# Kernel optimization log

Measured on AMD Instinct MI355X. Metric: run time of the kernel, lower is better.

The kernel has to match this reference:

```python
import jax, jax.numpy as jnp
import numpy as np

B, A, H, D, K = 131072, 6, 256, 128, 512
BETA = 0.25
VQ_LOSS_WEIGHT = 1.0


def setup_inputs() -> dict:
    key = jax.random.key(0)
    ks = jax.random.split(key, 16)
    s = 0.05
    inp = {
        "action": jax.random.normal(ks[0], (B, A), jnp.float32),
        # encoder: Linear(A,H)+ReLU, Linear(H,H)+ReLU, Linear(H,D)
        "enc1_w": jax.random.normal(ks[1], (H, A), jnp.float32) * s,
        "enc1_b": jnp.zeros((H,), jnp.float32),
        "enc2_w": jax.random.normal(ks[2], (H, H), jnp.float32) * s,
        "enc2_b": jnp.zeros((H,), jnp.float32),
        "mu_w": jax.random.normal(ks[3], (D, H), jnp.float32) * s,
        "mu_b": jnp.zeros((D,), jnp.float32),
        # VQ codebook, uniform(-1/K, 1/K) as in torch init
        "emb": jax.random.uniform(ks[4], (K, D), jnp.float32, -1.0 / K, 1.0 / K),
        # decoder: Linear(D,H)+ReLU, Linear(H,H)+ReLU, Linear(H,A)+Tanh
        "dec1_w": jax.random.normal(ks[5], (H, D), jnp.float32) * s,
        "dec1_b": jnp.zeros((H,), jnp.float32),
        "dec2_w": jax.random.normal(ks[6], (H, H), jnp.float32) * s,
        "dec2_b": jnp.zeros((H,), jnp.float32),
        "rec_w": jax.random.normal(ks[7], (A, H), jnp.float32) * s,
        "rec_b": jnp.zeros((A,), jnp.float32),
    }
    return inp


def _lin(x, w, b):
    return x @ w.T + b


def reference(action, enc1_w, enc1_b, enc2_w, enc2_b, mu_w, mu_b, emb,
              dec1_w, dec1_b, dec2_w, dec2_b, rec_w, rec_b):
    sg = jax.lax.stop_gradient
    # encoder MLP -> (B, D)
    h = jax.nn.relu(_lin(action, enc1_w, enc1_b))
    h = jax.nn.relu(_lin(h, enc2_w, enc2_b))
    enc = _lin(h, mu_w, mu_b)
    # VQ: argmin over squared L2 distance (same argmin as torch.cdist p=2)
    d2 = (jnp.sum(enc * enc, axis=1, keepdims=True)
          - 2.0 * (enc @ emb.T)
          + jnp.sum(emb * emb, axis=1))  # (B, K)
    idx = jnp.argmin(d2, axis=-1)  # (B,)
    q = emb[idx]  # (B, D) gather == onehot @ emb
    commitment_loss = jnp.mean((enc - sg(q)) ** 2)
    embedding_loss = jnp.mean((q - sg(enc)) ** 2)
    vq_loss = BETA * commitment_loss + embedding_loss
    # straight-through estimator
    q_st = enc + sg(q - enc)
    # decoder MLP (decode_action_head + decode_common + recons_action_head)
    h = jax.nn.relu(_lin(q_st, dec1_w, dec1_b))
    h = jax.nn.relu(_lin(h, dec2_w, dec2_b))
    recons = jnp.tanh(_lin(h, rec_w, rec_b))
    recons_loss = jnp.mean((recons - action) ** 2)
    total_loss = recons_loss + VQ_LOSS_WEIGHT * vq_loss
    return idx, q_st, total_loss
```

## Files before the change

kernel.cpp:

```cpp
#include <hip/hip_runtime.h>
#include <hip/hip_bf16.h>

#define NB 131072
#define MARGINF 2e-6f
#define WS_E2 256
#define WS_MASK 768
#define WS_MASKW 4096
#define WS_BASE_BYTES ((768 + 4096) * 4)
#define WS_SPLIT_F 4864
#define OFF_W2 0
#define OFF_W3 131072
#define OFF_EMB 196608
#define OFF_D1 327680
#define OFF_D2 393216
#define OFF_RW 524288
#define SPLIT_TOTAL 532480

typedef __attribute__((ext_vector_type(8))) short short8v;
typedef __attribute__((ext_vector_type(4))) float f32x4;
typedef __attribute__((ext_vector_type(4))) unsigned short ushort4v;

#define SWC(j) ((((j) >> 2) & 7) << 2)

__device__ __forceinline__ unsigned short bf16rn(float x) {
    unsigned u = __float_as_uint(x);
    unsigned r = u + 0x7fffu + ((u >> 16) & 1u);
    return (unsigned short)(r >> 16);
}
__device__ __forceinline__ void split2(float x, unsigned short& h, unsigned short& l) {
    h = bf16rn(x);
    float hf = __uint_as_float((unsigned)h << 16);
    l = bf16rn(x - hf);
}

__global__ void prep_kernel(
    const float* __restrict__ w2, const float* __restrict__ w3,
    const float* __restrict__ emb, const float* __restrict__ d1w,
    const float* __restrict__ d2w, const float* __restrict__ rw,
    float* __restrict__ ws, int do_splits)
{
    const int total = 512 + 266240;
    unsigned short* wsb = (unsigned short*)(ws + WS_SPLIT_F);
    for (int idx = blockIdx.x * 256 + threadIdx.x; idx < total; idx += gridDim.x * 256) {
        if (idx < 512) {
            const float* e = emb + (size_t)idx * 128;
            float s0 = 0.f, s1 = 0.f, s2 = 0.f, s3 = 0.f;
            for (int d = 0; d < 128; d += 4) {
                s0 += e[d] * e[d];     s1 += e[d + 1] * e[d + 1];
                s2 += e[d + 2] * e[d + 2]; s3 += e[d + 3] * e[d + 3];
            }
            ws[WS_E2 + idx] = (s0 + s1) + (s2 + s3);
            continue;
        }
        if (!do_splits) continue;
        int j = idx - 512;
        int base, K, o, k;
        float src;
        if (j < 65536) {
            o = j >> 8; k = j & 255; base = OFF_W2; K = 256; src = w2[o * 256 + k];
        } else if (j < 98304) {
            j -= 65536; o = j >> 8; k = j & 255; base = OFF_W3; K = 256; src = w3[o * 256 + k];
        } else if (j < 163840) {
            j -= 98304; o = j >> 7; k = j & 127; base = OFF_EMB; K = 128; src = emb[o * 128 + k];
        } else if (j < 196608) {
            j -= 163840; o = j >> 7; k = j & 127; base = OFF_D1; K = 128; src = d1w[o * 128 + k];
        } else if (j < 262144) {
            j -= 196608; o = j >> 8; k = j & 255; base = OFF_D2; K = 256; src = d2w[o * 256 + k];
        } else {
            j -= 262144; o = j >> 8; k = j & 255; base = OFF_RW; K = 256;
            src = (o < 6) ? rw[o * 256 + k] : 0.f;
        }
        unsigned short h, l;
        split2(src, h, l);
        int jt = o >> 4, c = k >> 5;
        int lane = (((k >> 3) & 3) << 4) | (o & 15);
        int e = k & 7;
        int a = base + ((jt * (K >> 5) + c) * 2) * 512 + lane * 8 + e;
        wsb[a] = h;
        wsb[a + 512] = l;
    }
}


template<int NJT, int KC, bool RELU, bool SQSUM>
__device__ __forceinline__ void mfma_mlp4(
    const short8v* __restrict__ Wf, const float* __restrict__ bias,
    unsigned short* HHp, unsigned short* HLp, float* ENC2Wp,
    int w, int lane)
{
    const int lc = lane & 15, lg = lane >> 4;
    f32x4 acc[NJT][4];
#pragma unroll
    for (int jj = 0; jj < NJT; ++jj)
#pragma unroll
        for (int rt = 0; rt < 4; ++rt)
            acc[jj][rt] = (f32x4){0.f, 0.f, 0.f, 0.f};

    __syncthreads();
    for (int c = 0; c < KC; ++c) {
        const int boff = c * 32 + lg * 8;
        short8v bh[4], bl[4];
#pragma unroll
        for (int rt = 0; rt < 4; ++rt) {
            bh[rt] = *(const short8v*)&HHp[(rt * 16 + lc) * 264 + boff];
            bl[rt] = *(const short8v*)&HLp[(rt * 16 + lc) * 264 + boff];
        }
#pragma unroll
        for (int jj = 0; jj < NJT; ++jj) {
            int fi = (((w * NJT + jj) * KC + c) * 2) * 64 + lane;
            short8v ah = Wf[fi];
            short8v al = Wf[fi + 64];
#pragma unroll
            for (int rt = 0; rt < 4; ++rt) {
                acc[jj][rt] = __builtin_amdgcn_mfma_f32_16x16x32_bf16(al, bh[rt], acc[jj][rt], 0, 0, 0);
                acc[jj][rt] = __builtin_amdgcn_mfma_f32_16x16x32_bf16(ah, bl[rt], acc[jj][rt], 0, 0, 0);
                acc[jj][rt] = __builtin_amdgcn_mfma_f32_16x16x32_bf16(ah, bh[rt], acc[jj][rt], 0, 0, 0);
            }
        }
    }
    __syncthreads();

    float sq[4] = {0.f, 0.f, 0.f, 0.f};
#pragma unroll
    for (int jj = 0; jj < NJT; ++jj) {
        int j0 = (w * NJT + jj) * 16 + lg * 4;
        float4 bv = *(const float4*)&bias[j0];
        float bb[4] = {bv.x, bv.y, bv.z, bv.w};
#pragma unroll
        for (int rt = 0; rt < 4; ++rt) {
            int r = rt * 16 + lc;
            ushort4v hv, lv;
#pragma unroll
            for (int reg = 0; reg < 4; ++reg) {
                float v = acc[jj][rt][reg] + bb[reg];
                if (RELU) v = fmaxf(v, 0.f);
                if (SQSUM) sq[rt] += v * v;
                unsigned short h, l;
                split2(v, h, l);
                hv[reg] = h; lv[reg] = l;
            }
            *(ushort4v*)&HHp[r * 264 + j0] = hv;
            *(ushort4v*)&HLp[r * 264 + j0] = lv;
        }
    }
    if (SQSUM) {
#pragma unroll
        for (int rt = 0; rt < 4; ++rt) {
            float s = sq[rt];
            s += __shfl_xor(s, 16);
            s += __shfl_xor(s, 32);
            if (lg == 0) ENC2Wp[w * 64 + rt * 16 + lc] = s;
        }
    }
}

__global__ __launch_bounds__(256, 2) void vqvae_main_mfma(
    const float* __restrict__ action,
    const float* __restrict__ w1, const float* __restrict__ b1,
    const float* __restrict__ b2, const float* __restrict__ b3,
    const float* __restrict__ emb,
    const float* __restrict__ d1b, const float* __restrict__ d2b,
    const float* __restrict__ rb,
    float* __restrict__ out, float* __restrict__ ws)
{
    extern __shared__ __align__(16) unsigned short DYN[];
    unsigned short* HH = DYN;
    unsigned short* HL = DYN + 64 * 264;

    __shared__ float AT[64 * 6];
    __shared__ float E2S[512];
    __shared__ float TOPV[4][64][3];
    __shared__ float ENC2W[4 * 64];
    __shared__ int IDXR[64];
    __shared__ int FLAGR[64];
    __shared__ float RED[8];

    const int t = threadIdx.x;
    const int w = t >> 6, lane = t & 63;
    const int lc = lane & 15, lg = lane >> 4;
    const int row0 = blockIdx.x * 64;
    const unsigned short* wsb = (const unsigned short*)(ws + WS_SPLIT_F);
    const short8v* W2f = (const short8v*)wsb + OFF_W2 / 8;
    const short8v* W3f = (const short8v*)wsb + OFF_W3 / 8;
    const short8v* EMBf = (const short8v*)wsb + OFF_EMB / 8;
    const short8v* D1f = (const short8v*)wsb + OFF_D1 / 8;
    const short8v* D2f = (const short8v*)wsb + OFF_D2 / 8;
    const short8v* RWf = (const short8v*)wsb + OFF_RW / 8;

    for (int i = t; i < 384; i += 256) AT[i] = action[(size_t)row0 * 6 + i];
    for (int i = t; i < 512; i += 256) E2S[i] = ws[WS_E2 + i];
    __syncthreads();

    {
        float wr[6];
#pragma unroll
        for (int i = 0; i < 6; ++i) wr[i] = w1[t * 6 + i];
        float bb = b1[t];
        for (int r = 0; r < 64; ++r) {
            float s = bb;
#pragma unroll
            for (int i = 0; i < 6; ++i) s += wr[i] * AT[r * 6 + i];
            s = fmaxf(s, 0.f);
            unsigned short h, l;
            split2(s, h, l);
            HH[r * 264 + t] = h;
            HL[r * 264 + t] = l;
        }
    }

    mfma_mlp4<4, 8, true, false>(W2f, b2, HH, HL, ENC2W, w, lane);
    mfma_mlp4<2, 8, false, true>(W3f, b3, HH, HL, ENC2W, w, lane);

    float lvq = 0.f, lrec = 0.f;
    {
        float v1[4][4], v2[4][4];
        int k1r[4][4];
#pragma unroll
        for (int rt = 0; rt < 4; ++rt)
#pragma unroll
            for (int reg = 0; reg < 4; ++reg) {
                v1[rt][reg] = 1e30f; v2[rt][reg] = 1e30f; k1r[rt][reg] = 0;
            }
        __syncthreads();
#pragma unroll
        for (int p = 0; p < 2; ++p) {
            f32x4 vacc[4][4];
#pragma unroll
            for (int kt = 0; kt < 4; ++kt)
#pragma unroll
                for (int rt = 0; rt < 4; ++rt)
                    vacc[kt][rt] = (f32x4){0.f, 0.f, 0.f, 0.f};
            for (int c = 0; c < 4; ++c) {
                const int aoff = c * 32 + lg * 8;
                short8v ah[4], al[4];
#pragma unroll
                for (int rt = 0; rt < 4; ++rt) {
                    ah[rt] = *(const short8v*)&HH[(rt * 16 + lc) * 264 + aoff];
                    al[rt] = *(const short8v*)&HL[(rt * 16 + lc) * 264 + aoff];
                }
#pragma unroll
                for (int kt = 0; kt < 4; ++kt) {
                    int ktg = w * 8 + p * 4 + kt;
                    int fi = ((ktg * 4 + c) * 2) * 64 + lane;
                    short8v bh = EMBf[fi];
                    short8v bl = EMBf[fi + 64];
#pragma unroll
                    for (int rt = 0; rt < 4; ++rt) {
                        vacc[kt][rt] = __builtin_amdgcn_mfma_f32_16x16x32_bf16(al[rt], bh, vacc[kt][rt], 0, 0, 0);
                        vacc[kt][rt] = __builtin_amdgcn_mfma_f32_16x16x32_bf16(ah[rt], bl, vacc[kt][rt], 0, 0, 0);
                        vacc[kt][rt] = __builtin_amdgcn_mfma_f32_16x16x32_bf16(ah[rt], bh, vacc[kt][rt], 0, 0, 0);
                    }
                }
            }
#pragma unroll
            for (int kt = 0; kt < 4; ++kt) {
                int k = (w * 8 + p * 4 + kt) * 16 + lc;
                float ek = E2S[k];
#pragma unroll
                for (int rt = 0; rt < 4; ++rt)
#pragma unroll
                    for (int reg = 0; reg < 4; ++reg) {
                        float dd = ek - 2.f * vacc[kt][rt][reg];
                        if (dd < v1[rt][reg]) {
                            v2[rt][reg] = v1[rt][reg]; v1[rt][reg] = dd; k1r[rt][reg] = k;
                        } else if (dd < v2[rt][reg]) v2[rt][reg] = dd;
                    }
            }
        }
        __syncthreads();

#pragma unroll
        for (int m = 1; m < 16; m <<= 1) {
#pragma unroll
            for (int rt = 0; rt < 4; ++rt)
#pragma unroll
                for (int reg = 0; reg < 4; ++reg) {
                    float ov1 = __shfl_xor(v1[rt][reg], m);
                    int ok1 = __shfl_xor(k1r[rt][reg], m);
                    float ov2 = __shfl_xor(v2[rt][reg], m);
                    if (ov1 < v1[rt][reg] ||
                        (ov1 == v1[rt][reg] && ok1 < k1r[rt][reg])) {
                        v2[rt][reg] = fminf(v1[rt][reg], ov2);
                        v1[rt][reg] = ov1; k1r[rt][reg] = ok1;
                    } else {
                        v2[rt][reg] = fminf(v2[rt][reg], ov1);
                    }
                }
        }
        if (lc == 0) {
#pragma unroll
            for (int rt = 0; rt < 4; ++rt)
#pragma unroll
                for (int reg = 0; reg < 4; ++reg) {
                    int row = rt * 16 + lg * 4 + reg;
                    TOPV[w][row][0] = v1[rt][reg];
                    TOPV[w][row][1] = __int_as_float(k1r[rt][reg]);
                    TOPV[w][row][2] = v2[rt][reg];
                }
        }
    }
    __syncthreads();

    if (t < 64) {
        float v1 = 1e30f, v2 = 1e30f; int k1 = 0;
#pragma unroll
        for (int ww = 0; ww < 4; ++ww) {
            float ov1 = TOPV[ww][t][0];
            int ok1 = __float_as_int(TOPV[ww][t][1]);
            float ov2 = TOPV[ww][t][2];
            if (ov1 < v1 || (ov1 == v1 && ok1 < k1)) {
                v2 = fminf(v1, ov2); v1 = ov1; k1 = ok1;
            } else {
                v2 = fminf(v2, ov1);
            }
        }
        int flag = (v2 - v1 >= MARGINF) ? 0 : 1;
        IDXR[t] = k1;
        FLAGR[t] = flag;
        int row = row0 + t;
        if (flag)
            atomicOr((unsigned int*)ws + WS_MASK + (row >> 5), 1u << (row & 31));
        out[row] = (float)k1;
        if (!flag) {
            float enc2 = ENC2W[0 * 64 + t] + ENC2W[1 * 64 + t] +
                         ENC2W[2 * 64 + t] + ENC2W[3 * 64 + t];
            lvq = enc2 + v1;
        }
    }
    __syncthreads();

    {
        int d = t & 127, rhalf = t >> 7;
#pragma unroll
        for (int e = 0; e < 32; ++e) {
            int r = (e << 1) | rhalf;
            int k1 = IDXR[r];
            float q = emb[(size_t)k1 * 128 + d];
            out[NB + (size_t)(row0 + r) * 128 + d] = q;
            unsigned short h, l;
            split2(q, h, l);
            HH[r * 264 + d] = h;
            HL[r * 264 + d] = l;
        }
    }

    mfma_mlp4<4, 4, true, false>(D1f, d1b, HH, HL, ENC2W, w, lane);
    mfma_mlp4<4, 8, true, false>(D2f, d2b, HH, HL, ENC2W, w, lane);
    __syncthreads();

    {
        f32x4 racc = (f32x4){0.f, 0.f, 0.f, 0.f};
        for (int c = 0; c < 8; ++c) {
            const int boff = c * 32 + lg * 8;
            short8v bh = *(const short8v*)&HH[(w * 16 + lc) * 264 + boff];
            short8v bl = *(const short8v*)&HL[(w * 16 + lc) * 264 + boff];
            int fi = (c * 2) * 64 + lane;
            short8v ah = RWf[fi];
            short8v al = RWf[fi + 64];
            racc = __builtin_amdgcn_mfma_f32_16x16x32_bf16(al, bh, racc, 0, 0, 0);
            racc = __builtin_amdgcn_mfma_f32_16x16x32_bf16(ah, bl, racc, 0, 0, 0);
            racc = __builtin_amdgcn_mfma_f32_16x16x32_bf16(ah, bh, racc, 0, 0, 0);
        }
        int r = w * 16 + lc;
#pragma unroll
        for (int reg = 0; reg < 4; ++reg) {
            int j = lg * 4 + reg;
            if (j < 6) {
                float rec = tanhf(racc[reg] + rb[j]);
                float df = rec - AT[r * 6 + j];
                if (!FLAGR[r]) lrec += df * df;
            }
        }
    }

#pragma unroll
    for (int m = 1; m < 64; m <<= 1) {
        lvq += __shfl_xor(lvq, m);
        lrec += __shfl_xor(lrec, m);
    }
    if ((t & 63) == 0) { RED[t >> 6] = lvq; RED[4 + (t >> 6)] = lrec; }
    __syncthreads();
    if (t == 0) {
        int slot = blockIdx.x & 63;
        atomicAdd((double*)ws + slot, (double)((RED[0] + RED[1]) + (RED[2] + RED[3])));
        atomicAdd((double*)ws + 64 + slot, (double)((RED[4] + RED[5]) + (RED[6] + RED[7])));
    }
}

__global__ __launch_bounds__(256) void vqvae_fix(
    const float* __restrict__ action,
    const float* __restrict__ w1, const float* __restrict__ b1,
    const float* __restrict__ w2, const float* __restrict__ b2,
    const float* __restrict__ w3, const float* __restrict__ b3,
    const float* __restrict__ emb,
    const float* __restrict__ d1w, const float* __restrict__ d1b,
    const float* __restrict__ d2w, const float* __restrict__ d2b,
    const float* __restrict__ rw, const float* __restrict__ rb,
    float* __restrict__ out, float* __restrict__ ws)
{
    __shared__ double H1[256];
    __shared__ double H2[256];
    __shared__ double ENC[128];
    __shared__ double QD[128];
    __shared__ double SRED[256];
    __shared__ int SK[256];
    __shared__ double SA[6];

    const int t = threadIdx.x;
    const unsigned int word = ((const unsigned int*)ws)[WS_MASK + blockIdx.x];
    if (word == 0u) return;

    for (int bit = 0; bit < 32; ++bit) {
        if (!(word & (1u << bit))) continue;
        const int row = (blockIdx.x << 5) + bit;

        if (t < 6) SA[t] = (double)action[(size_t)row * 6 + t];
        __syncthreads();
        {
            double a = (double)b1[t];
#pragma unroll
            for (int i = 0; i < 6; ++i) a += (double)w1[t * 6 + i] * SA[i];
            H1[t] = a > 0.0 ? a : 0.0;
        }
        __syncthreads();
        {
            const float* w = w2 + (size_t)t * 256;
            double a0 = 0, a1 = 0, a2 = 0, a3 = 0;
            for (int i = 0; i < 256; i += 4) {
                a0 += (double)w[i] * H1[i];     a1 += (double)w[i + 1] * H1[i + 1];
                a2 += (double)w[i + 2] * H1[i + 2]; a3 += (double)w[i + 3] * H1[i + 3];
            }
            double a = (double)b2[t] + a0 + a1 + a2 + a3;
            H2[t] = a > 0.0 ? a : 0.0;
        }
        __syncthreads();
        if (t < 128) {
            const float* w = w3 + (size_t)t * 256;
            double a0 = 0, a1 = 0, a2 = 0, a3 = 0;
            for (int i = 0; i < 256; i += 4) {
                a0 += (double)w[i] * H2[i];     a1 += (double)w[i + 1] * H2[i + 1];
                a2 += (double)w[i + 2] * H2[i + 2]; a3 += (double)w[i + 3] * H2[i + 3];
            }
            ENC[t] = (double)b3[t] + a0 + a1 + a2 + a3;
        }
        __syncthreads();
        double best = 1e300; int bk = 0;
#pragma unroll
        for (int kk = 0; kk < 2; ++kk) {
            int k = t + kk * 256;
            const float* e = emb + (size_t)k * 128;
            double s0 = 0, s1 = 0;
            for (int d = 0; d < 128; d += 2) {
                double df0 = ENC[d] - (double)e[d];
                double df1 = ENC[d + 1] - (double)e[d + 1];
                s0 += df0 * df0; s1 += df1 * df1;
            }
            double s = s0 + s1;
            if (s < best) { best = s; bk = k; }
        }
        SRED[t] = best; SK[t] = bk;
        __syncthreads();
        for (int st = 128; st > 0; st >>= 1) {
            if (t < st) {
                double ov = SRED[t + st]; int ok = SK[t + st];
                if (ov < SRED[t] || (ov == SRED[t] && ok < SK[t])) { SRED[t] = ov; SK[t] = ok; }
            }
            __syncthreads();
        }
        const int bestk = SK[0];
        double lv = 0.0;
        if (t < 128) {
            double q = (double)emb[(size_t)bestk * 128 + t];
            QD[t] = q;
            double df = ENC[t] - q;
            lv = df * df;
            out[NB + (size_t)row * 128 + t] = (float)q;
        }
        if (t == 0) out[row] = (float)bestk;
        __syncthreads();
        {
            const float* w = d1w + (size_t)t * 128;
            double a0 = 0, a1 = 0;
            for (int i = 0; i < 128; i += 2) {
                a0 += (double)w[i] * QD[i]; a1 += (double)w[i + 1] * QD[i + 1];
            }
            double a = (double)d1b[t] + a0 + a1;
            H1[t] = a > 0.0 ? a : 0.0;
        }
        __syncthreads();
        {
            const float* w = d2w + (size_t)t * 256;
            double a0 = 0, a1 = 0, a2 = 0, a3 = 0;
            for (int i = 0; i < 256; i += 4) {
                a0 += (double)w[i] * H1[i];     a1 += (double)w[i + 1] * H1[i + 1];
                a2 += (double)w[i + 2] * H1[i + 2]; a3 += (double)w[i + 3] * H1[i + 3];
            }
            double a = (double)d2b[t] + a0 + a1 + a2 + a3;
            H2[t] = a > 0.0 ? a : 0.0;
        }
        __syncthreads();
        double lr = 0.0;
        if (t < 6) {
            const float* w = rw + (size_t)t * 256;
            double a0 = 0, a1 = 0;
            for (int i = 0; i < 256; i += 2) {
                a0 += (double)w[i] * H2[i]; a1 += (double)w[i + 1] * H2[i + 1];
            }
            double rec = tanh((double)rb[t] + a0 + a1);
            double df = rec - SA[t];
            lr = df * df;
        }
        SRED[t] = lv;
        __syncthreads();
        for (int st = 128; st > 0; st >>= 1) {
            if (t < st) SRED[t] += SRED[t + st];
            __syncthreads();
        }
        if (t == 0) atomicAdd((double*)ws + 0, SRED[0]);
        if (t < 6) atomicAdd((double*)ws + 64, lr);
        __syncthreads();
    }
}

__global__ void vqvae_fin(const float* __restrict__ ws, float* __restrict__ out) {
    if (threadIdx.x == 0 && blockIdx.x == 0) {
        const double* D = (const double*)ws;
        double sv = 0.0, sr = 0.0;
        for (int i = 0; i < 64; ++i) { sv += D[i]; sr += D[64 + i]; }
        double loss = sr / ((double)NB * 6.0) + 1.25 * (sv / ((double)NB * 128.0));
        out[(size_t)NB * 129] = (float)loss;
    }
}

static __device__ __forceinline__ void gemm_out256(
    const float* __restrict__ W, const float* __restrict__ bias, int IN,
    const float* __restrict__ hin, float* __restrict__ hout,
    float* __restrict__ WC, int t, int tx, int r0, bool do_relu)
{
    float acc[2][4][4];
#pragma unroll
    for (int g = 0; g < 2; ++g)
#pragma unroll
        for (int a = 0; a < 4; ++a)
#pragma unroll
            for (int b = 0; b < 4; ++b) acc[g][a][b] = 0.f;
    float4 pa = *(const float4*)(W + (size_t)t * IN);
    float4 pb = *(const float4*)(W + (size_t)t * IN + 4);
    for (int i0 = 0; i0 < IN; i0 += 8) {
        __syncthreads();
        WC[0 * 256 + t] = pa.x; WC[1 * 256 + t] = pa.y;
        WC[2 * 256 + t] = pa.z; WC[3 * 256 + t] = pa.w;
        WC[4 * 256 + t] = pb.x; WC[5 * 256 + t] = pb.y;
        WC[6 * 256 + t] = pb.z; WC[7 * 256 + t] = pb.w;
        __syncthreads();
        if (i0 + 8 < IN) {
            pa = *(const float4*)(W + (size_t)t * IN + i0 + 8);
            pb = *(const float4*)(W + (size_t)t * IN + i0 + 12);
        }
#pragma unroll
        for (int i = 0; i < 8; ++i) {
            int row = i0 + i;
            float4 h = *(const float4*)&hin[row * 32 + (r0 ^ SWC(row))];
            float4 w0 = *(const float4*)&WC[i * 256 + 4 * tx];
            float4 w1v = *(const float4*)&WC[i * 256 + 128 + 4 * tx];
            float wv0[4] = {w0.x, w0.y, w0.z, w0.w};
            float wv1[4] = {w1v.x, w1v.y, w1v.z, w1v.w};
            float hv[4] = {h.x, h.y, h.z, h.w};
#pragma unroll
            for (int a = 0; a < 4; ++a)
#pragma unroll
                for (int b = 0; b < 4; ++b) {
                    acc[0][a][b] += wv0[a] * hv[b];
                    acc[1][a][b] += wv1[a] * hv[b];
                }
        }
    }
#pragma unroll
    for (int g = 0; g < 2; ++g)
#pragma unroll
        for (int a = 0; a < 4; ++a) {
            int j = g * 128 + 4 * tx + a;
            float bj = bias[j];
            float4 v;
            v.x = acc[g][a][0] + bj; v.y = acc[g][a][1] + bj;
            v.z = acc[g][a][2] + bj; v.w = acc[g][a][3] + bj;
            if (do_relu) {
                v.x = fmaxf(v.x, 0.f); v.y = fmaxf(v.y, 0.f);
                v.z = fmaxf(v.z, 0.f); v.w = fmaxf(v.w, 0.f);
            }
            *(float4*)&hout[j * 32 + (r0 ^ SWC(j))] = v;
        }
    __syncthreads();
}

__global__ __launch_bounds__(256, 2) void vqvae_main_fp32(
    const float* __restrict__ action,
    const float* __restrict__ w1, const float* __restrict__ b1,
    const float* __restrict__ w2, const float* __restrict__ b2,
    const float* __restrict__ w3, const float* __restrict__ b3,
    const float* __restrict__ emb,
    const float* __restrict__ d1w, const float* __restrict__ d1b,
    const float* __restrict__ d2w, const float* __restrict__ d2b,
    const float* __restrict__ rw, const float* __restrict__ rb,
    float* __restrict__ out, float* __restrict__ ws)
{
    __shared__ float X[256 * 32];
    __shared__ float Y[256 * 32];
    __shared__ float WC[2048];
    __shared__ float AT[6 * 32];
    __shared__ int IDXR[32];
    __shared__ int FLAGR[32];
    __shared__ float RED[8];

    const int t = threadIdx.x;
    const int tx = t & 31, ty = t >> 5;
    const int r0 = ty * 4;
    const int row0 = blockIdx.x * 32;

    if (t < 192) {
        int r = t / 6, i = t - r * 6;
        AT[i * 32 + r] = action[(size_t)row0 * 6 + t];
    }
    __syncthreads();
    {
#pragma unroll
        for (int i = 0; i < 6; ++i) WC[i * 256 + t] = w1[t * 6 + i];
        __syncthreads();
        float acc[2][4][4];
#pragma unroll
        for (int g = 0; g < 2; ++g)
#pragma unroll
            for (int a = 0; a < 4; ++a)
#pragma unroll
                for (int b = 0; b < 4; ++b) acc[g][a][b] = 0.f;
#pragma unroll
        for (int i = 0; i < 6; ++i) {
            float4 h = *(const float4*)&AT[i * 32 + r0];
            float4 w0 = *(const float4*)&WC[i * 256 + 4 * tx];
            float4 w1v = *(const float4*)&WC[i * 256 + 128 + 4 * tx];
            float wv0[4] = {w0.x, w0.y, w0.z, w0.w};
            float wv1[4] = {w1v.x, w1v.y, w1v.z, w1v.w};
            float hv[4] = {h.x, h.y, h.z, h.w};
#pragma unroll
            for (int a = 0; a < 4; ++a)
#pragma unroll
                for (int b = 0; b < 4; ++b) {
                    acc[0][a][b] += wv0[a] * hv[b];
                    acc[1][a][b] += wv1[a] * hv[b];
                }
        }
#pragma unroll
        for (int g = 0; g < 2; ++g)
#pragma unroll
            for (int a = 0; a < 4; ++a) {
                int j = g * 128 + 4 * tx + a;
                float bj = b1[j];
                float4 v;
                v.x = fmaxf(acc[g][a][0] + bj, 0.f);
                v.y = fmaxf(acc[g][a][1] + bj, 0.f);
                v.z = fmaxf(acc[g][a][2] + bj, 0.f);
                v.w = fmaxf(acc[g][a][3] + bj, 0.f);
                *(float4*)&X[j * 32 + (r0 ^ SWC(j))] = v;
            }
        __syncthreads();
    }
    gemm_out256(w2, b2, 256, X, Y, WC, t, tx, r0, true);
    {
        float acc[4][4];
#pragma unroll
        for (int a = 0; a < 4; ++a)
#pragma unroll
            for (int b = 0; b < 4; ++b) acc[a][b] = 0.f;
        float4 pa, pb;
        if (t < 128) {
            pa = *(const float4*)(w3 + (size_t)t * 256);
            pb = *(const float4*)(w3 + (size_t)t * 256 + 4);
        }
        for (int i0 = 0; i0 < 256; i0 += 8) {
            __syncthreads();
            if (t < 128) {
                WC[0 * 128 + t] = pa.x; WC[1 * 128 + t] = pa.y;
                WC[2 * 128 + t] = pa.z; WC[3 * 128 + t] = pa.w;
                WC[4 * 128 + t] = pb.x; WC[5 * 128 + t] = pb.y;
                WC[6 * 128 + t] = pb.z; WC[7 * 128 + t] = pb.w;
            }
            __syncthreads();
            if (t < 128 && i0 + 8 < 256) {
                pa = *(const float4*)(w3 + (size_t)t * 256 + i0 + 8);
                pb = *(const float4*)(w3 + (size_t)t * 256 + i0 + 12);
            }
#pragma unroll
            for (int i = 0; i < 8; ++i) {
                int row = i0 + i;
                float4 h = *(const float4*)&Y[row * 32 + (r0 ^ SWC(row))];
                float4 w0 = *(const float4*)&WC[i * 128 + 4 * tx];
                float wv[4] = {w0.x, w0.y, w0.z, w0.w};
                float hv[4] = {h.x, h.y, h.z, h.w};
#pragma unroll
                for (int a = 0; a < 4; ++a)
#pragma unroll
                    for (int b = 0; b < 4; ++b) acc[a][b] += wv[a] * hv[b];
            }
        }
#pragma unroll
        for (int a = 0; a < 4; ++a) {
            int j = 4 * tx + a;
            float bj = b3[j];
            float4 v;
            v.x = acc[a][0] + bj; v.y = acc[a][1] + bj;
            v.z = acc[a][2] + bj; v.w = acc[a][3] + bj;
            *(float4*)&X[j * 32 + (r0 ^ SWC(j))] = v;
        }
        __syncthreads();
    }
    {
        float bv1[4], bv2[4];
        int bk1[4];
        float acc[4][4][4];
#pragma unroll
        for (int p = 0; p < 4; ++p)
#pragma unroll
            for (int a = 0; a < 4; ++a)
#pragma unroll
                for (int b = 0; b < 4; ++b) acc[p][a][b] = 0.f;
        float4 qa = *(const float4*)(emb + (size_t)t * 128);
        float4 qb = *(const float4*)(emb + (size_t)(t + 256) * 128);
        for (int d0 = 0; d0 < 128; d0 += 4) {
            __syncthreads();
            WC[0 * 512 + t] = qa.x; WC[1 * 512 + t] = qa.y;
            WC[2 * 512 + t] = qa.z; WC[3 * 512 + t] = qa.w;
            WC[0 * 512 + 256 + t] = qb.x; WC[1 * 512 + 256 + t] = qb.y;
            WC[2 * 512 + 256 + t] = qb.z; WC[3 * 512 + 256 + t] = qb.w;
            __syncthreads();
            if (d0 + 4 < 128) {
                qa = *(const float4*)(emb + (size_t)t * 128 + d0 + 4);
                qb = *(const float4*)(emb + (size_t)(t + 256) * 128 + d0 + 4);
            }
#pragma unroll
            for (int i = 0; i < 4; ++i) {
                int row = d0 + i;
                float4 h = *(const float4*)&X[row * 32 + (r0 ^ SWC(row))];
                float hv[4] = {h.x, h.y, h.z, h.w};
#pragma unroll
                for (int p = 0; p < 4; ++p) {
                    float4 w0 = *(const float4*)&WC[i * 512 + p * 128 + 4 * tx];
                    float wv[4] = {w0.x, w0.y, w0.z, w0.w};
#pragma unroll
                    for (int a = 0; a < 4; ++a)
#pragma unroll
                        for (int b = 0; b < 4; ++b) acc[p][a][b] += wv[a] * hv[b];
                }
            }
        }
#pragma unroll
        for (int b = 0; b < 4; ++b) { bv1[b] = 1e30f; bv2[b] = 1e30f; bk1[b] = 0; }
#pragma unroll
        for (int p = 0; p < 4; ++p)
#pragma unroll
            for (int a = 0; a < 4; ++a) {
                int k = p * 128 + 4 * tx + a;
                float ek = ws[WS_E2 + k];
#pragma unroll
                for (int b = 0; b < 4; ++b) {
                    float dd = ek - 2.f * acc[p][a][b];
                    if (dd < bv1[b]) { bv2[b] = bv1[b]; bv1[b] = dd; bk1[b] = k; }
                    else if (dd < bv2[b]) bv2[b] = dd;
                }
            }
#pragma unroll
        for (int m = 1; m < 32; m <<= 1) {
#pragma unroll
            for (int b = 0; b < 4; ++b) {
                float ov1 = __shfl_xor(bv1[b], m);
                int ok1 = __shfl_xor(bk1[b], m);
                float ov2 = __shfl_xor(bv2[b], m);
                if (ov1 < bv1[b] || (ov1 == bv1[b] && ok1 < bk1[b])) {
                    bv2[b] = fminf(bv1[b], ov2);
                    bv1[b] = ov1; bk1[b] = ok1;
                } else {
                    bv2[b] = fminf(bv2[b], ov1);
                }
            }
        }
        if (tx == 0) {
#pragma unroll
            for (int b = 0; b < 4; ++b) {
                IDXR[r0 + b] = bk1[b];
                FLAGR[r0 + b] = (bv2[b] - bv1[b] >= MARGINF) ? 0 : 1;
            }
        }
    }
    __syncthreads();
    if (t < 32) {
        int row = row0 + t;
        if (FLAGR[t])
            atomicOr((unsigned int*)ws + WS_MASK + (row >> 5), 1u << (row & 31));
        out[row] = (float)IDXR[t];
    }
    float lvq = 0.f, lrec = 0.f;
    {
        int d = t & 127, rq = t >> 7;
        int cd = SWC(d);
#pragma unroll
        for (int e = 0; e < 4; ++e) {
            int rr = (rq + 2 * e) * 4;
            float4 en = *(const float4*)&X[d * 32 + (rr ^ cd)];
            float q0 = emb[(size_t)IDXR[rr + 0] * 128 + d];
            float q1 = emb[(size_t)IDXR[rr + 1] * 128 + d];
            float q2 = emb[(size_t)IDXR[rr + 2] * 128 + d];
            float q3 = emb[(size_t)IDXR[rr + 3] * 128 + d];
            float4 qv; qv.x = q0; qv.y = q1; qv.z = q2; qv.w = q3;
            *(float4*)&X[(128 + d) * 32 + (rr ^ cd)] = qv;
            if (!FLAGR[rr + 0]) lvq += (en.x - q0) * (en.x - q0);
            if (!FLAGR[rr + 1]) lvq += (en.y - q1) * (en.y - q1);
            if (!FLAGR[rr + 2]) lvq += (en.z - q2) * (en.z - q2);
            if (!FLAGR[rr + 3]) lvq += (en.w - q3) * (en.w - q3);
            out[NB + (size_t)(row0 + rr + 0) * 128 + d] = q0;
            out[NB + (size_t)(row0 + rr + 1) * 128 + d] = q1;
            out[NB + (size_t)(row0 + rr + 2) * 128 + d] = q2;
            out[NB + (size_t)(row0 + rr + 3) * 128 + d] = q3;
        }
    }
    __syncthreads();
    gemm_out256(d1w, d1b, 128, X + 128 * 32, Y, WC, t, tx, r0, true);
    gemm_out256(d2w, d2b, 256, Y, X, WC, t, tx, r0, true);
    if (t < 192) {
        int jj = t >> 5, r = t & 31;
        const float* wr = rw + jj * 256;
        float a0 = 0.f, a1 = 0.f, a2 = 0.f, a3 = 0.f;
        for (int i = 0; i < 256; i += 4) {
            a0 += wr[i] * X[i * 32 + (r ^ SWC(i))];
            a1 += wr[i + 1] * X[(i + 1) * 32 + (r ^ SWC(i + 1))];
            a2 += wr[i + 2] * X[(i + 2) * 32 + (r ^ SWC(i + 2))];
            a3 += wr[i + 3] * X[(i + 3) * 32 + (r ^ SWC(i + 3))];
        }
        float rec = tanhf(rb[jj] + (a0 + a1) + (a2 + a3));
        float df = rec - AT[jj * 32 + r];
        if (!FLAGR[r]) lrec = df * df;
    }
#pragma unroll
    for (int m = 1; m < 64; m <<= 1) {
        lvq += __shfl_xor(lvq, m);
        lrec += __shfl_xor(lrec, m);
    }
    if ((t & 63) == 0) { RED[t >> 6] = lvq; RED[4 + (t >> 6)] = lrec; }
    __syncthreads();
    if (t == 0) {
        int slot = blockIdx.x & 63;
        atomicAdd((double*)ws + slot, (double)((RED[0] + RED[1]) + (RED[2] + RED[3])));
        atomicAdd((double*)ws + 64 + slot, (double)((RED[4] + RED[5]) + (RED[6] + RED[7])));
    }
}

extern "C" void kernel_launch(void* const* d_in, const int* in_sizes, int n_in,
                              void* d_out, int out_size, void* d_ws, size_t ws_size,
                              hipStream_t stream) {
    const float* action = (const float*)d_in[0];
    const float* w1 = (const float*)d_in[1];
    const float* b1 = (const float*)d_in[2];
    const float* w2 = (const float*)d_in[3];
    const float* b2 = (const float*)d_in[4];
    const float* w3 = (const float*)d_in[5];
    const float* b3 = (const float*)d_in[6];
    const float* emb = (const float*)d_in[7];
    const float* d1w = (const float*)d_in[8];
    const float* d1b = (const float*)d_in[9];
    const float* d2w = (const float*)d_in[10];
    const float* d2b = (const float*)d_in[11];
    const float* rw = (const float*)d_in[12];
    const float* rb = (const float*)d_in[13];
    float* out = (float*)d_out;
    float* ws = (float*)d_ws;

    const size_t need_mfma = (size_t)WS_BASE_BYTES + (size_t)SPLIT_TOTAL * 2;
    const int use_mfma = (ws_size >= need_mfma) ? 1 : 0;
    const int dyn_lds = 64 * 264 * 2 * 2;

    size_t clear = ws_size < (size_t)WS_BASE_BYTES ? ws_size : (size_t)WS_BASE_BYTES;
    hipMemsetAsync(d_ws, 0, clear, stream);

    prep_kernel<<<1043, 256, 0, stream>>>(w2, w3, emb, d1w, d2w, rw, ws, use_mfma);
    if (use_mfma) {
        hipFuncSetAttribute((const void*)vqvae_main_mfma,
                            hipFuncAttributeMaxDynamicSharedMemorySize, dyn_lds);
        vqvae_main_mfma<<<NB / 64, 256, dyn_lds, stream>>>(action, w1, b1, b2, b3, emb,
                                                           d1b, d2b, rb, out, ws);
    } else {
        vqvae_main_fp32<<<NB / 32, 256, 0, stream>>>(action, w1, b1, w2, b2, w3, b3, emb,
                                                     d1w, d1b, d2w, d2b, rw, rb, out, ws);
    }
    vqvae_fix<<<NB / 32, 256, 0, stream>>>(action, w1, b1, w2, b2, w3, b3, emb,
                                           d1w, d1b, d2w, d2b, rw, rb, out, ws);
    vqvae_fin<<<1, 64, 0, stream>>>(ws, out);
}
```

Measured before the change: 480.3 us.

## Use single-term bf16 MFMA in decoder and tighten fallback margin, grid-stride fix kernel

The decoder layers (dec1, dec2, recon) now use a single bf16×bf16 MFMA term instead of the three-term hi/lo split-precision emulation, and store only the high bf16 half of activations. This cuts decoder MFMA work and LDS traffic roughly threefold, at the cost of lower precision in the reconstruction loss. The near-tie margin that sends rows to the fp64 fix path is tightened, so fewer rows are recomputed. The fix kernel now launches 256 blocks that grid-stride over the mask words, replacing one block per word, so most blocks no longer launch just to exit.

```diff
diff --git a/kernel.cpp b/kernel.cpp
--- a/kernel.cpp
+++ b/kernel.cpp
@@ -2,7 +2,7 @@
 #include <hip/hip_bf16.h>
 
 #define NB 131072
-#define MARGINF 2e-6f
+#define MARGINF 5e-7f
 #define WS_E2 256
 #define WS_MASK 768
 #define WS_MASKW 4096
@@ -82,7 +82,7 @@
 }
 
 
-template<int NJT, int KC, bool RELU, bool SQSUM>
+template<int NJT, int KC, bool RELU, bool SQSUM, int TERMS, bool WRITELO>
 __device__ __forceinline__ void mfma_mlp4(
     const short8v* __restrict__ Wf, const float* __restrict__ bias,
     unsigned short* HHp, unsigned short* HLp, float* ENC2Wp,
@@ -103,18 +103,25 @@
 #pragma unroll
         for (int rt = 0; rt < 4; ++rt) {
             bh[rt] = *(const short8v*)&HHp[(rt * 16 + lc) * 264 + boff];
-            bl[rt] = *(const short8v*)&HLp[(rt * 16 + lc) * 264 + boff];
+            if (TERMS == 3)
+                bl[rt] = *(const short8v*)&HLp[(rt * 16 + lc) * 264 + boff];
         }
 #pragma unroll
         for (int jj = 0; jj < NJT; ++jj) {
             int fi = (((w * NJT + jj) * KC + c) * 2) * 64 + lane;
             short8v ah = Wf[fi];
-            short8v al = Wf[fi + 64];
-#pragma unroll
-            for (int rt = 0; rt < 4; ++rt) {
-                acc[jj][rt] = __builtin_amdgcn_mfma_f32_16x16x32_bf16(al, bh[rt], acc[jj][rt], 0, 0, 0);
-                acc[jj][rt] = __builtin_amdgcn_mfma_f32_16x16x32_bf16(ah, bl[rt], acc[jj][rt], 0, 0, 0);
-                acc[jj][rt] = __builtin_amdgcn_mfma_f32_16x16x32_bf16(ah, bh[rt], acc[jj][rt], 0, 0, 0);
+            if (TERMS == 3) {
+                short8v al = Wf[fi + 64];
+#pragma unroll
+                for (int rt = 0; rt < 4; ++rt) {
+                    acc[jj][rt] = __builtin_amdgcn_mfma_f32_16x16x32_bf16(al, bh[rt], acc[jj][rt], 0, 0, 0);
+                    acc[jj][rt] = __builtin_amdgcn_mfma_f32_16x16x32_bf16(ah, bl[rt], acc[jj][rt], 0, 0, 0);
+                    acc[jj][rt] = __builtin_amdgcn_mfma_f32_16x16x32_bf16(ah, bh[rt], acc[jj][rt], 0, 0, 0);
+                }
+            } else {
+#pragma unroll
+                for (int rt = 0; rt < 4; ++rt)
+                    acc[jj][rt] = __builtin_amdgcn_mfma_f32_16x16x32_bf16(ah, bh[rt], acc[jj][rt], 0, 0, 0);
             }
         }
     }
@@ -135,12 +142,16 @@
                 float v = acc[jj][rt][reg] + bb[reg];
                 if (RELU) v = fmaxf(v, 0.f);
                 if (SQSUM) sq[rt] += v * v;
-                unsigned short h, l;
-                split2(v, h, l);
-                hv[reg] = h; lv[reg] = l;
+                if (WRITELO) {
+                    unsigned short h, l;
+                    split2(v, h, l);
+                    hv[reg] = h; lv[reg] = l;
+                } else {
+                    hv[reg] = bf16rn(v);
+                }
             }
             *(ushort4v*)&HHp[r * 264 + j0] = hv;
-            *(ushort4v*)&HLp[r * 264 + j0] = lv;
+            if (WRITELO) *(ushort4v*)&HLp[r * 264 + j0] = lv;
         }
     }
     if (SQSUM) {
@@ -208,8 +219,8 @@
         }
     }
 
-    mfma_mlp4<4, 8, true, false>(W2f, b2, HH, HL, ENC2W, w, lane);
-    mfma_mlp4<2, 8, false, true>(W3f, b3, HH, HL, ENC2W, w, lane);
+    mfma_mlp4<4, 8, true, false, 3, true>(W2f, b2, HH, HL, ENC2W, w, lane);
+    mfma_mlp4<2, 8, false, true, 3, true>(W3f, b3, HH, HL, ENC2W, w, lane);
 
     float lvq = 0.f, lrec = 0.f;
     {
@@ -337,15 +348,12 @@
             int k1 = IDXR[r];
             float q = emb[(size_t)k1 * 128 + d];
             out[NB + (size_t)(row0 + r) * 128 + d] = q;
-            unsigned short h, l;
-            split2(q, h, l);
-            HH[r * 264 + d] = h;
-            HL[r * 264 + d] = l;
-        }
-    }
-
-    mfma_mlp4<4, 4, true, false>(D1f, d1b, HH, HL, ENC2W, w, lane);
-    mfma_mlp4<4, 8, true, false>(D2f, d2b, HH, HL, ENC2W, w, lane);
+            HH[r * 264 + d] = bf16rn(q);
+        }
+    }
+
+    mfma_mlp4<4, 4, true, false, 1, false>(D1f, d1b, HH, HL, ENC2W, w, lane);
+    mfma_mlp4<4, 8, true, false, 1, false>(D2f, d2b, HH, HL, ENC2W, w, lane);
     __syncthreads();
 
     {
@@ -353,12 +361,8 @@
         for (int c = 0; c < 8; ++c) {
             const int boff = c * 32 + lg * 8;
             short8v bh = *(const short8v*)&HH[(w * 16 + lc) * 264 + boff];
-            short8v bl = *(const short8v*)&HL[(w * 16 + lc) * 264 + boff];
             int fi = (c * 2) * 64 + lane;
             short8v ah = RWf[fi];
-            short8v al = RWf[fi + 64];
-            racc = __builtin_amdgcn_mfma_f32_16x16x32_bf16(al, bh, racc, 0, 0, 0);
-            racc = __builtin_amdgcn_mfma_f32_16x16x32_bf16(ah, bl, racc, 0, 0, 0);
             racc = __builtin_amdgcn_mfma_f32_16x16x32_bf16(ah, bh, racc, 0, 0, 0);
         }
         int r = w * 16 + lc;
@@ -407,118 +411,121 @@
     __shared__ double SA[6];
 
     const int t = threadIdx.x;
-    const unsigned int word = ((const unsigned int*)ws)[WS_MASK + blockIdx.x];
-    if (word == 0u) return;
-
-    for (int bit = 0; bit < 32; ++bit) {
-        if (!(word & (1u << bit))) continue;
-        const int row = (blockIdx.x << 5) + bit;
-
-        if (t < 6) SA[t] = (double)action[(size_t)row * 6 + t];
-        __syncthreads();
-        {
-            double a = (double)b1[t];
-#pragma unroll
-            for (int i = 0; i < 6; ++i) a += (double)w1[t * 6 + i] * SA[i];
-            H1[t] = a > 0.0 ? a : 0.0;
-        }
-        __syncthreads();
-        {
-            const float* w = w2 + (size_t)t * 256;
-            double a0 = 0, a1 = 0, a2 = 0, a3 = 0;
-            for (int i = 0; i < 256; i += 4) {
-                a0 += (double)w[i] * H1[i];     a1 += (double)w[i + 1] * H1[i + 1];
-                a2 += (double)w[i + 2] * H1[i + 2]; a3 += (double)w[i + 3] * H1[i + 3];
-            }
-            double a = (double)b2[t] + a0 + a1 + a2 + a3;
-            H2[t] = a > 0.0 ? a : 0.0;
-        }
-        __syncthreads();
-        if (t < 128) {
-            const float* w = w3 + (size_t)t * 256;
-            double a0 = 0, a1 = 0, a2 = 0, a3 = 0;
-            for (int i = 0; i < 256; i += 4) {
-                a0 += (double)w[i] * H2[i];     a1 += (double)w[i + 1] * H2[i + 1];
-                a2 += (double)w[i + 2] * H2[i + 2]; a3 += (double)w[i + 3] * H2[i + 3];
-            }
-            ENC[t] = (double)b3[t] + a0 + a1 + a2 + a3;
-        }
-        __syncthreads();
-        double best = 1e300; int bk = 0;
-#pragma unroll
-        for (int kk = 0; kk < 2; ++kk) {
-            int k = t + kk * 256;
-            const float* e = emb + (size_t)k * 128;
-            double s0 = 0, s1 = 0;
-            for (int d = 0; d < 128; d += 2) {
-                double df0 = ENC[d] - (double)e[d];
-                double df1 = ENC[d + 1] - (double)e[d + 1];
-                s0 += df0 * df0; s1 += df1 * df1;
-            }
-            double s = s0 + s1;
-            if (s < best) { best = s; bk = k; }
-        }
-        SRED[t] = best; SK[t] = bk;
-        __syncthreads();
-        for (int st = 128; st > 0; st >>= 1) {
-            if (t < st) {
-                double ov = SRED[t + st]; int ok = SK[t + st];
-                if (ov < SRED[t] || (ov == SRED[t] && ok < SK[t])) { SRED[t] = ov; SK[t] = ok; }
-            }
-            __syncthreads();
-        }
-        const int bestk = SK[0];
-        double lv = 0.0;
-        if (t < 128) {
-            double q = (double)emb[(size_t)bestk * 128 + t];
-            QD[t] = q;
-            double df = ENC[t] - q;
-            lv = df * df;
-            out[NB + (size_t)row * 128 + t] = (float)q;
-        }
-        if (t == 0) out[row] = (float)bestk;
-        __syncthreads();
-        {
-            const float* w = d1w + (size_t)t * 128;
-            double a0 = 0, a1 = 0;
-            for (int i = 0; i < 128; i += 2) {
-                a0 += (double)w[i] * QD[i]; a1 += (double)w[i + 1] * QD[i + 1];
-            }
-            double a = (double)d1b[t] + a0 + a1;
-            H1[t] = a > 0.0 ? a : 0.0;
-        }
-        __syncthreads();
-        {
-            const float* w = d2w + (size_t)t * 256;
-            double a0 = 0, a1 = 0, a2 = 0, a3 = 0;
-            for (int i = 0; i < 256; i += 4) {
-                a0 += (double)w[i] * H1[i];     a1 += (double)w[i + 1] * H1[i + 1];
-                a2 += (double)w[i + 2] * H1[i + 2]; a3 += (double)w[i + 3] * H1[i + 3];
-            }
-            double a = (double)d2b[t] + a0 + a1 + a2 + a3;
-            H2[t] = a > 0.0 ? a : 0.0;
-        }
-        __syncthreads();
-        double lr = 0.0;
-        if (t < 6) {
-            const float* w = rw + (size_t)t * 256;
-            double a0 = 0, a1 = 0;
-            for (int i = 0; i < 256; i += 2) {
-                a0 += (double)w[i] * H2[i]; a1 += (double)w[i + 1] * H2[i + 1];
-            }
-            double rec = tanh((double)rb[t] + a0 + a1);
-            double df = rec - SA[t];
-            lr = df * df;
-        }
-        SRED[t] = lv;
-        __syncthreads();
-        for (int st = 128; st > 0; st >>= 1) {
-            if (t < st) SRED[t] += SRED[t + st];
-            __syncthreads();
-        }
-        if (t == 0) atomicAdd((double*)ws + 0, SRED[0]);
-        if (t < 6) atomicAdd((double*)ws + 64, lr);
-        __syncthreads();
+
+    for (int widx = blockIdx.x; widx < WS_MASKW; widx += gridDim.x) {
+        const unsigned int word = ((const unsigned int*)ws)[WS_MASK + widx];
+        if (word == 0u) continue;
+
+        for (int bit = 0; bit < 32; ++bit) {
+            if (!(word & (1u << bit))) continue;
+            const int row = (widx << 5) + bit;
+
+            if (t < 6) SA[t] = (double)action[(size_t)row * 6 + t];
+            __syncthreads();
+            {
+                double a = (double)b1[t];
+#pragma unroll
+                for (int i = 0; i < 6; ++i) a += (double)w1[t * 6 + i] * SA[i];
+                H1[t] = a > 0.0 ? a : 0.0;
+            }
+            __syncthreads();
+            {
+                const float* w = w2 + (size_t)t * 256;
+                double a0 = 0, a1 = 0, a2 = 0, a3 = 0;
+                for (int i = 0; i < 256; i += 4) {
+                    a0 += (double)w[i] * H1[i];     a1 += (double)w[i + 1] * H1[i + 1];
+                    a2 += (double)w[i + 2] * H1[i + 2]; a3 += (double)w[i + 3] * H1[i + 3];
+                }
+                double a = (double)b2[t] + a0 + a1 + a2 + a3;
+                H2[t] = a > 0.0 ? a : 0.0;
+            }
+            __syncthreads();
+            if (t < 128) {
+                const float* w = w3 + (size_t)t * 256;
+                double a0 = 0, a1 = 0, a2 = 0, a3 = 0;
+                for (int i = 0; i < 256; i += 4) {
+                    a0 += (double)w[i] * H2[i];     a1 += (double)w[i + 1] * H2[i + 1];
+                    a2 += (double)w[i + 2] * H2[i + 2]; a3 += (double)w[i + 3] * H2[i + 3];
+                }
+                ENC[t] = (double)b3[t] + a0 + a1 + a2 + a3;
+            }
+            __syncthreads();
+            double best = 1e300; int bk = 0;
+#pragma unroll
+            for (int kk = 0; kk < 2; ++kk) {
+                int k = t + kk * 256;
+                const float* e = emb + (size_t)k * 128;
+                double s0 = 0, s1 = 0;
+                for (int d = 0; d < 128; d += 2) {
+                    double df0 = ENC[d] - (double)e[d];
+                    double df1 = ENC[d + 1] - (double)e[d + 1];
+                    s0 += df0 * df0; s1 += df1 * df1;
+                }
+                double s = s0 + s1;
+                if (s < best) { best = s; bk = k; }
+            }
+            SRED[t] = best; SK[t] = bk;
+            __syncthreads();
+            for (int st = 128; st > 0; st >>= 1) {
+                if (t < st) {
+                    double ov = SRED[t + st]; int ok = SK[t + st];
+                    if (ov < SRED[t] || (ov == SRED[t] && ok < SK[t])) { SRED[t] = ov; SK[t] = ok; }
+                }
+                __syncthreads();
+            }
+            const int bestk = SK[0];
+            double lv = 0.0;
+            if (t < 128) {
+                double q = (double)emb[(size_t)bestk * 128 + t];
+                QD[t] = q;
+                double df = ENC[t] - q;
+                lv = df * df;
+                out[NB + (size_t)row * 128 + t] = (float)q;
+            }
+            if (t == 0) out[row] = (float)bestk;
+            __syncthreads();
+            {
+                const float* w = d1w + (size_t)t * 128;
+                double a0 = 0, a1 = 0;
+                for (int i = 0; i < 128; i += 2) {
+                    a0 += (double)w[i] * QD[i]; a1 += (double)w[i + 1] * QD[i + 1];
+                }
+                double a = (double)d1b[t] + a0 + a1;
+                H1[t] = a > 0.0 ? a : 0.0;
+            }
+            __syncthreads();
+            {
+                const float* w = d2w + (size_t)t * 256;
+                double a0 = 0, a1 = 0, a2 = 0, a3 = 0;
+                for (int i = 0; i < 256; i += 4) {
+                    a0 += (double)w[i] * H1[i];     a1 += (double)w[i + 1] * H1[i + 1];
+                    a2 += (double)w[i + 2] * H1[i + 2]; a3 += (double)w[i + 3] * H1[i + 3];
+                }
+                double a = (double)d2b[t] + a0 + a1 + a2 + a3;
+                H2[t] = a > 0.0 ? a : 0.0;
+            }
+            __syncthreads();
+            double lr = 0.0;
+            if (t < 6) {
+                const float* w = rw + (size_t)t * 256;
+                double a0 = 0, a1 = 0;
+                for (int i = 0; i < 256; i += 2) {
+                    a0 += (double)w[i] * H2[i]; a1 += (double)w[i + 1] * H2[i + 1];
+                }
+                double rec = tanh((double)rb[t] + a0 + a1);
+                double df = rec - SA[t];
+                lr = df * df;
+            }
+            SRED[t] = lv;
+            __syncthreads();
+            for (int st = 128; st > 0; st >>= 1) {
+                if (t < st) SRED[t] += SRED[t + st];
+                __syncthreads();
+            }
+            if (t == 0) atomicAdd((double*)ws + 0, SRED[0]);
+            if (t < 6) atomicAdd((double*)ws + 64, lr);
+            __syncthreads();
+        }
     }
 }
 
@@ -889,7 +896,7 @@
         vqvae_main_fp32<<<NB / 32, 256, 0, stream>>>(action, w1, b1, w2, b2, w3, b3, emb,
                                                      d1w, d1b, d2w, d2b, rw, rb, out, ws);
     }
-    vqvae_fix<<<NB / 32, 256, 0, stream>>>(action, w1, b1, w2, b2, w3, b3, emb,
-                                           d1w, d1b, d2w, d2b, rw, rb, out, ws);
+    vqvae_fix<<<256, 256, 0, stream>>>(action, w1, b1, w2, b2, w3, b3, emb,
+                                       d1w, d1b, d2w, d2b, rw, rb, out, ws);
     vqvae_fin<<<1, 64, 0, stream>>>(ws, out);
 }
```

Result: faster. 395.6 us (-17.6%).
